# Performance work log

Hardware: AMD Instinct MI355X
Metric: run time of the kernel (lower is better)

## Reference

```python
import jax, jax.numpy as jnp
import numpy as np

EMBED_DIM = 128
NUM_SYMBOLS = 200000
B = 1024
K = 200
PROCESS_STEPS = 4


def setup_inputs() -> dict:
    key = jax.random.key(0)
    ks = jax.random.split(key, 10)
    D = EMBED_DIM
    emb = jax.random.normal(ks[0], (NUM_SYMBOLS + 1, D), jnp.float32) * 0.02
    emb = emb.at[NUM_SYMBOLS].set(0.0)  # padding_idx row
    return {
        "relations": jax.random.randint(ks[1], (B, K), 0, NUM_SYMBOLS),
        "entities": jax.random.randint(ks[2], (B, K), 0, NUM_SYMBOLS),
        "query": jax.random.randint(ks[3], (B,), 0, NUM_SYMBOLS),
        "symbol_emb": emb,
        "gcn_w_w": jax.random.normal(ks[4], (D, 2 * D), jnp.float32) / np.sqrt(2 * D).astype(np.float32),
        "gcn_w_b": jnp.zeros((D,), jnp.float32),
        "p1_w": jax.random.normal(ks[5], (2 * D, D), jnp.float32) / np.sqrt(D).astype(np.float32),
        "p1_b": jnp.zeros((2 * D,), jnp.float32),
        "p2_w": jax.random.normal(ks[6], (D, 2 * D), jnp.float32) / np.sqrt(2 * D).astype(np.float32),
        "p2_b": jnp.zeros((D,), jnp.float32),
        "ln_a": jnp.ones((D,), jnp.float32),
        "ln_b": jnp.zeros((D,), jnp.float32),
        "w_ih": jax.random.normal(ks[7], (8 * D, D), jnp.float32) * 0.05,
        "w_hh": jax.random.normal(ks[8], (8 * D, 2 * D), jnp.float32) * 0.05,
        "b_ih": jnp.zeros((8 * D,), jnp.float32),
        "b_hh": jnp.zeros((8 * D,), jnp.float32),
    }


def _layer_norm(z, a, b, eps=1e-3):
    # repo's LayerNormalization: (z - mu) / (std + eps) * a + b, unbiased std
    mu = jnp.mean(z, axis=-1, keepdims=True)
    sigma = jnp.std(z, axis=-1, ddof=1, keepdims=True)
    return (z - mu) / (sigma + eps) * a + b


def _forward(symbol_emb, gcn_w_w, gcn_w_b, p1_w, p1_b, p2_w, p2_b,
             ln_a, ln_b, w_ih, w_hh, b_ih, b_hh,
             relations, entities, query):
    D = symbol_emb.shape[1]
    # --- neighbor_encoder: gather -> concat -> linear -> neighbor sum -> tanh
    rel_e = symbol_emb[relations]                       # (B, K, D)
    ent_e = symbol_emb[entities]                        # (B, K, D)
    concat = jnp.concatenate([rel_e, ent_e], axis=-1)   # (B, K, 2D)
    out = jnp.einsum('bkf,df->bkd', concat, gcn_w_w) + gcn_w_b
    num_neighbors = jnp.asarray(relations.shape[0], out.dtype)  # code uses relations.size()[0]
    support = jnp.tanh(out.sum(axis=1) / num_neighbors)  # (B, D)
    # --- SupportEncoder: FFN with residual + layernorm (dropout off in eval)
    hidden = jax.nn.relu(support @ p1_w.T + p1_b)        # (B, 2D)
    support_g = _layer_norm(hidden @ p2_w.T + p2_b + support, ln_a, ln_b)
    # --- QueryEncoder: LSTMCell(D, 2D) process block with attention over support
    q = symbol_emb[query]                                # (B, D)
    bsz = q.shape[0]
    h_r = jnp.zeros((bsz, 2 * D), q.dtype)
    c = jnp.zeros((bsz, 2 * D), q.dtype)
    h_out = q
    for _ in range(PROCESS_STEPS):
        gates = q @ w_ih.T + b_ih + h_r @ w_hh.T + b_hh  # (B, 8D)
        i, f, g, o = jnp.split(gates, 4, axis=-1)
        c = jax.nn.sigmoid(f) * c + jax.nn.sigmoid(i) * jnp.tanh(g)
        h_ = jax.nn.sigmoid(o) * jnp.tanh(c)             # (B, 2D)
        h_out = q + h_[:, :D]                            # (B, D)
        attn = jax.nn.softmax(h_out @ support_g.T, axis=1)  # (B, B)
        r = attn @ support_g                             # (B, D)
        h_r = jnp.concatenate([h_out, r], axis=-1)       # (B, 2D)
    query_embeds = h_out
    # --- cosine similarity over dim=1
    cross = jnp.sum(query_embeds * support_g, axis=1)
    n1 = jnp.sum(query_embeds * query_embeds, axis=1)
    n2 = jnp.sum(support_g * support_g, axis=1)
    return cross / jnp.sqrt(n1 * n2)                     # (B,)


def reference(relations, entities, query, symbol_emb, gcn_w_w, gcn_w_b,
              p1_w, p1_b, p2_w, p2_b, ln_a, ln_b, w_ih, w_hh, b_ih, b_hh):
    return _forward(symbol_emb, gcn_w_w, gcn_w_b, p1_w, p1_b, p2_w, p2_b,
                    ln_a, ln_b, w_ih, w_hh, b_ih, b_hh,
                    relations, entities, query)
```

## Files before the change

### kernel.cpp

```cpp
#include <hip/hip_runtime.h>
#include <math.h>

#define D 128
#define B_SZ 1024
#define KNB 200
#define AHW 392
#define PW 1048

typedef _Float16 half8 __attribute__((ext_vector_type(8)));
typedef float floatx4 __attribute__((ext_vector_type(4)));

__device__ __forceinline__ float sigmoid_f(float x) { return 1.f / (1.f + __expf(-x)); }
__device__ __forceinline__ float tanh_fast(float x) { return 1.f - 2.f / (__expf(2.f * x) + 1.f); }

__device__ __forceinline__ half8 h8zero() {
    half8 z;
    #pragma unroll
    for (int i = 0; i < 8; ++i) z[i] = (_Float16)0.f;
    return z;
}

__global__ __launch_bounds__(512) void k_support(
    const int* __restrict__ relations, const int* __restrict__ entities,
    const int* __restrict__ query, const float* __restrict__ emb,
    const float* __restrict__ gcn_w, const float* __restrict__ gcn_b,
    const float* __restrict__ p1_w, const float* __restrict__ p1_b,
    const float* __restrict__ p2_w, const float* __restrict__ p2_b,
    const float* __restrict__ ln_a, const float* __restrict__ ln_b,
    const float* __restrict__ w_ih, const float* __restrict__ w_hh,
    _Float16* __restrict__ w16,
    float* __restrict__ sg, _Float16* __restrict__ sgH, _Float16* __restrict__ sgT,
    float* __restrict__ qb, _Float16* __restrict__ qbH)
{
    __shared__ int idxs[2 * KNB];
    __shared__ __align__(16) float part[16][132];
    __shared__ __align__(16) float S[2 * D];
    __shared__ __align__(16) float sup[D];
    __shared__ __align__(16) float hid[2 * D];
    __shared__ __align__(16) float zv[D];
    __shared__ float red2[2];

    const int b = blockIdx.x;
    const int t = threadIdx.x;

    if (b < 96) {
        const int i8 = (b * 512 + t) * 8;
        const float* src = (i8 < 131072) ? (w_ih + i8) : (w_hh + (i8 - 131072));
        float4 v0 = *(const float4*)src;
        float4 v1 = *(const float4*)(src + 4);
        half8 h;
        h[0] = (_Float16)v0.x; h[1] = (_Float16)v0.y; h[2] = (_Float16)v0.z; h[3] = (_Float16)v0.w;
        h[4] = (_Float16)v1.x; h[5] = (_Float16)v1.y; h[6] = (_Float16)v1.z; h[7] = (_Float16)v1.w;
        *(half8*)&w16[i8] = h;
    }

    if (t < KNB) idxs[t] = relations[b * KNB + t];
    else if (t < 2 * KNB) idxs[t] = entities[b * KNB + (t - KNB)];
    __syncthreads();

    {
        const int g = t >> 5, c4 = (t & 31) * 4;
        const int* mi = &idxs[(g >> 3) * KNB];
        float4 a4 = make_float4(0.f, 0.f, 0.f, 0.f);
        #pragma unroll 5
        for (int k = (g & 7); k < KNB; k += 8) {
            float4 v = *(const float4*)&emb[(size_t)mi[k] * D + c4];
            a4.x += v.x; a4.y += v.y; a4.z += v.z; a4.w += v.w;
        }
        *(float4*)&part[g][c4] = a4;
    }
    __syncthreads();
    if (t < 2 * D) {
        const int half = t >> 7, c = t & 127;
        float s = 0.f;
        #pragma unroll
        for (int j = 0; j < 8; ++j) s += part[half * 8 + j][c];
        S[t] = s;
    }
    __syncthreads();

    if (t < D) {
        const float4* w4 = (const float4*)(gcn_w + t * 2 * D);
        float dot = 0.f;
        #pragma unroll 8
        for (int f = 0; f < 2 * D / 4; ++f) {
            float4 w = w4[f];
            float4 s = *(const float4*)&S[f * 4];
            dot += w.x * s.x + w.y * s.y + w.z * s.z + w.w * s.w;
        }
        float v = (dot + 200.f * gcn_b[t]) * (1.f / 1024.f);
        sup[t] = tanhf(v);
    }
    __syncthreads();

    if (t < 2 * D) {
        const float4* w4 = (const float4*)(p1_w + t * D);
        float dot = 0.f;
        #pragma unroll 8
        for (int f = 0; f < D / 4; ++f) {
            float4 w = w4[f];
            float4 s = *(const float4*)&sup[f * 4];
            dot += w.x * s.x + w.y * s.y + w.z * s.z + w.w * s.w;
        }
        float h = dot + p1_b[t];
        hid[t] = h > 0.f ? h : 0.f;
    }
    __syncthreads();

    if (t < D) {
        const float4* w4 = (const float4*)(p2_w + t * 2 * D);
        float dot = 0.f;
        #pragma unroll 8
        for (int f = 0; f < 2 * D / 4; ++f) {
            float4 w = w4[f];
            float4 s = *(const float4*)&hid[f * 4];
            dot += w.x * s.x + w.y * s.y + w.z * s.z + w.w * s.w;
        }
        zv[t] = dot + p2_b[t] + sup[t];
    }
    __syncthreads();

    if (t < 64) {
        float x0 = zv[t], x1 = zv[t + 64];
        float s = x0 + x1;
        for (int off = 32; off; off >>= 1) s += __shfl_down(s, off);
        float mu = __shfl(s, 0) * (1.f / 128.f);
        float d0 = x0 - mu, d1 = x1 - mu;
        float v = d0 * d0 + d1 * d1;
        for (int off = 32; off; off >>= 1) v += __shfl_down(v, off);
        v = __shfl(v, 0);
        if (t == 0) { red2[0] = mu; red2[1] = sqrtf(v * (1.f / 127.f)); }
    }
    __syncthreads();
    if (t < D) {
        float mu = red2[0], sigma = red2[1];
        float val = (zv[t] - mu) / (sigma + 1e-3f) * ln_a[t] + ln_b[t];
        sg[b * D + t] = val;
        sgH[b * D + t] = (_Float16)val;
        sgT[t * B_SZ + b] = (_Float16)val;
        float qv = emb[(size_t)query[b] * D + t];
        qb[b * D + t] = qv;
        qbH[b * D + t] = (_Float16)qv;
    }
}

__global__ __launch_bounds__(512)
void k_lstm(
    const _Float16* __restrict__ qbH, const float* __restrict__ qb,
    const _Float16* __restrict__ sgH, const _Float16* __restrict__ sgT,
    const float* __restrict__ sg, const _Float16* __restrict__ w16,
    const float* __restrict__ b_ih, const float* __restrict__ b_hh,
    float* __restrict__ out)
{
    __shared__ _Float16 Ah[16 * AHW];
    __shared__ _Float16 P[16 * PW];
    __shared__ float qF[8][132];
    __shared__ float hF[8][132];
    __shared__ float pm[8][12];
    __shared__ float ps[8][12];

    const int t = threadIdx.x;
    const int w = t >> 6, lane = t & 63;
    const int m = lane & 15, quad = lane >> 4;
    const int b0 = blockIdx.x * 8;

    for (int i = t; i < 16 * AHW / 8; i += 512) *(half8*)&Ah[i * 8] = h8zero();
    for (int i = t; i < 8 * PW / 8; i += 512) *(half8*)&P[8 * PW + i * 8] = h8zero();
    __syncthreads();
    if (t < 128) {
        const int row = t >> 4, c = (t & 15) * 8;
        *(half8*)&Ah[row * AHW + c] = *(const half8*)&qbH[(size_t)(b0 + row) * D + c];
    }
    if (t < 256) {
        const int row = t >> 5, c = (t & 31) * 4;
        *(float4*)&qF[row][c] = *(const float4*)&qb[(size_t)(b0 + row) * D + c];
    }
    __syncthreads();

    float cregA[4] = {0.f, 0.f, 0.f, 0.f};
    float cregB[4] = {0.f, 0.f, 0.f, 0.f};

    #pragma unroll 1
    for (int s = 0; s < 4; ++s) {
        if (s > 0) {
            floatx4 a2[8];
            #pragma unroll
            for (int i = 0; i < 8; ++i)
                #pragma unroll
                for (int z = 0; z < 4; ++z) a2[i][z] = 0.f;
            #pragma unroll 1
            for (int ks = 0; ks < 4; ++ks) {
                half8 a = *(const half8*)&Ah[m * AHW + 128 + ks * 32 + quad * 8];
                const _Float16* sb = sgH + (size_t)m * D + ks * 32 + quad * 8;
                #pragma unroll
                for (int g4 = 0; g4 < 2; ++g4) {
                    half8 b0v = *(const half8*)(sb + (size_t)((w * 8 + g4 * 4 + 0) * 16) * D);
                    half8 b1v = *(const half8*)(sb + (size_t)((w * 8 + g4 * 4 + 1) * 16) * D);
                    half8 b2v = *(const half8*)(sb + (size_t)((w * 8 + g4 * 4 + 2) * 16) * D);
                    half8 b3v = *(const half8*)(sb + (size_t)((w * 8 + g4 * 4 + 3) * 16) * D);
                    a2[g4 * 4 + 0] = __builtin_amdgcn_mfma_f32_16x16x32_f16(a, b0v, a2[g4 * 4 + 0], 0, 0, 0);
                    a2[g4 * 4 + 1] = __builtin_amdgcn_mfma_f32_16x16x32_f16(a, b1v, a2[g4 * 4 + 1], 0, 0, 0);
                    a2[g4 * 4 + 2] = __builtin_amdgcn_mfma_f32_16x16x32_f16(a, b2v, a2[g4 * 4 + 2], 0, 0, 0);
                    a2[g4 * 4 + 3] = __builtin_amdgcn_mfma_f32_16x16x32_f16(a, b3v, a2[g4 * 4 + 3], 0, 0, 0);
                }
            }

            float mx[4];
            #pragma unroll
            for (int rr = 0; rr < 4; ++rr) {
                float v0 = fmaxf(fmaxf(a2[0][rr], a2[1][rr]), fmaxf(a2[2][rr], a2[3][rr]));
                float v1 = fmaxf(fmaxf(a2[4][rr], a2[5][rr]), fmaxf(a2[6][rr], a2[7][rr]));
                mx[rr] = fmaxf(v0, v1);
            }
            #pragma unroll
            for (int off = 1; off <= 8; off <<= 1)
                #pragma unroll
                for (int rr = 0; rr < 4; ++rr)
                    mx[rr] = fmaxf(mx[rr], __shfl_xor(mx[rr], off));
            if (m == 0) {
                #pragma unroll
                for (int rr = 0; rr < 4; ++rr) {
                    const int row = quad * 4 + rr;
                    if (row < 8) pm[w][row] = mx[rr];
                }
            }
            __syncthreads();

            float gm[4];
            #pragma unroll
            for (int rr = 0; rr < 4; ++rr) {
                const int row = quad * 4 + rr;
                float mm = -1e30f;
                if (row < 8) {
                    #pragma unroll
                    for (int ww = 0; ww < 8; ++ww) mm = fmaxf(mm, pm[ww][row]);
                }
                gm[rr] = mm;
            }
            float sl[4] = {0.f, 0.f, 0.f, 0.f};
            #pragma unroll
            for (int i = 0; i < 8; ++i) {
                const int col = (w * 8 + i) * 16 + m;
                #pragma unroll
                for (int rr = 0; rr < 4; ++rr) {
                    const int row = quad * 4 + rr;
                    if (row < 8) {
                        float e = __expf(a2[i][rr] - gm[rr]);
                        P[row * PW + col] = (_Float16)e;
                        sl[rr] += e;
                    }
                }
            }
            #pragma unroll
            for (int off = 1; off <= 8; off <<= 1)
                #pragma unroll
                for (int rr = 0; rr < 4; ++rr)
                    sl[rr] += __shfl_xor(sl[rr], off);
            if (m == 0) {
                #pragma unroll
                for (int rr = 0; rr < 4; ++rr) {
                    const int row = quad * 4 + rr;
                    if (row < 8) ps[w][row] = sl[rr];
                }
            }
            __syncthreads();

            float sinvd[4];
            #pragma unroll
            for (int rr = 0; rr < 4; ++rr) {
                const int row = quad * 4 + rr;
                float ss = 1.f;
                if (row < 8) {
                    ss = 0.f;
                    #pragma unroll
                    for (int ww = 0; ww < 8; ++ww) ss += ps[ww][row];
                }
                sinvd[rr] = 1.f / ss;
            }

            {
                floatx4 a3;
                #pragma unroll
                for (int z = 0; z < 4; ++z) a3[z] = 0.f;
                const _Float16* tb = sgT + (size_t)(w * 16 + m) * B_SZ + quad * 8;
                half8 c0 = *(const half8*)(tb);
                half8 c1 = *(const half8*)(tb + 32);
                #pragma unroll 1
                for (int ks = 0; ks < 32; ++ks) {
                    half8 nx = c1;
                    if (ks < 30) nx = *(const half8*)(tb + (ks + 2) * 32);
                    half8 a = *(const half8*)&P[m * PW + ks * 32 + quad * 8];
                    a3 = __builtin_amdgcn_mfma_f32_16x16x32_f16(a, c0, a3, 0, 0, 0);
                    c0 = c1; c1 = nx;
                }
                #pragma unroll
                for (int rr = 0; rr < 4; ++rr) {
                    const int row = quad * 4 + rr;
                    if (row < 8)
                        Ah[row * AHW + 256 + w * 16 + m] = (_Float16)(a3[rr] * sinvd[rr]);
                }
            }
            __syncthreads();
        }

        float hreg[4] = {0.f, 0.f, 0.f, 0.f};
        auto gates_half = [&](int v, float* cregH, bool wantH) {
            floatx4 acc[4];
            #pragma unroll
            for (int g = 0; g < 4; ++g) {
                floatx4 ac;
                #pragma unroll
                for (int z = 0; z < 4; ++z) ac[z] = 0.f;
                const _Float16* wb0 = w16 + (size_t)(g * 256 + v * 16 + m) * 128 + quad * 8;
                const _Float16* wb1 = w16 + 131072 + (size_t)(g * 256 + v * 16 + m) * 256 + quad * 8;
                half8 cur = *(const half8*)wb0;
                #pragma unroll 1
                for (int ks = 0; ks < 12; ++ks) {
                    half8 nxt = cur;
                    if (ks < 3)       nxt = *(const half8*)(wb0 + (ks + 1) * 32);
                    else if (ks < 11) nxt = *(const half8*)(wb1 + (ks - 3) * 32);
                    half8 a = *(const half8*)&Ah[m * AHW + ks * 32 + quad * 8];
                    ac = __builtin_amdgcn_mfma_f32_16x16x32_f16(a, cur, ac, 0, 0, 0);
                    cur = nxt;
                }
                acc[g] = ac;
            }
            const int unit = v * 16 + m;
            float bi0 = b_ih[unit] + b_hh[unit];
            float bi1 = b_ih[256 + unit] + b_hh[256 + unit];
            float bi2 = b_ih[512 + unit] + b_hh[512 + unit];
            float bi3 = b_ih[768 + unit] + b_hh[768 + unit];
            #pragma unroll
            for (int rr = 0; rr < 4; ++rr) {
                float gi = acc[0][rr] + bi0;
                float gf = acc[1][rr] + bi1;
                float gg = acc[2][rr] + bi2;
                float go = acc[3][rr] + bi3;
                float cn = sigmoid_f(gf) * cregH[rr] + sigmoid_f(gi) * tanh_fast(gg);
                cregH[rr] = cn;
                if (wantH) hreg[rr] = sigmoid_f(go) * tanh_fast(cn);
            }
        };
        gates_half(w, cregA, true);
        gates_half(w + 8, cregB, false);
        __syncthreads();

        {
            const int unit = w * 16 + m;
            #pragma unroll
            for (int rr = 0; rr < 4; ++rr) {
                const int row = quad * 4 + rr;
                if (row < 8) {
                    float ho = qF[row][unit] + hreg[rr];
                    Ah[row * AHW + 128 + unit] = (_Float16)ho;
                    hF[row][unit] = ho;
                }
            }
        }
        __syncthreads();
    }

    {
        const int row = w;
        float a0 = hF[row][lane], a1 = hF[row][lane + 64];
        float s0 = sg[(size_t)(b0 + row) * D + lane], s1 = sg[(size_t)(b0 + row) * D + lane + 64];
        float cr = a0 * s0 + a1 * s1;
        float n1 = a0 * a0 + a1 * a1;
        float n2 = s0 * s0 + s1 * s1;
        for (int off = 32; off; off >>= 1) {
            cr += __shfl_down(cr, off);
            n1 += __shfl_down(n1, off);
            n2 += __shfl_down(n2, off);
        }
        if (lane == 0) out[b0 + row] = cr / sqrtf(n1 * n2);
    }
}

extern "C" void kernel_launch(void* const* d_in, const int* in_sizes, int n_in,
                              void* d_out, int out_size, void* d_ws, size_t ws_size,
                              hipStream_t stream)
{
    const int*   relations = (const int*)d_in[0];
    const int*   entities  = (const int*)d_in[1];
    const int*   query     = (const int*)d_in[2];
    const float* emb       = (const float*)d_in[3];
    const float* gcn_w     = (const float*)d_in[4];
    const float* gcn_b     = (const float*)d_in[5];
    const float* p1_w      = (const float*)d_in[6];
    const float* p1_b      = (const float*)d_in[7];
    const float* p2_w      = (const float*)d_in[8];
    const float* p2_b      = (const float*)d_in[9];
    const float* ln_a      = (const float*)d_in[10];
    const float* ln_b      = (const float*)d_in[11];
    const float* w_ih      = (const float*)d_in[12];
    const float* w_hh      = (const float*)d_in[13];
    const float* b_ih      = (const float*)d_in[14];
    const float* b_hh      = (const float*)d_in[15];

    float* ws = (float*)d_ws;
    float*     sg   = ws;
    float*     qb   = ws + 131072;
    _Float16*  sgH  = (_Float16*)(ws + 262144);
    _Float16*  sgT  = (_Float16*)(ws + 327680);
    _Float16*  qbH  = (_Float16*)(ws + 393216);
    _Float16*  w16  = (_Float16*)(ws + 458752);

    k_support<<<dim3(B_SZ), dim3(512), 0, stream>>>(
        relations, entities, query, emb, gcn_w, gcn_b,
        p1_w, p1_b, p2_w, p2_b, ln_a, ln_b,
        w_ih, w_hh, w16,
        sg, sgH, sgT, qb, qbH);
    k_lstm<<<dim3(B_SZ / 8), dim3(512), 0, stream>>>(
        qbH, qb, sgH, sgT, sg, w16, b_ih, b_hh, (float*)d_out);
}
```

Before: 328.0 us.

## Interleave fused W_ih/W_hh weights and software-pipeline LSTM MFMA loops

The fp16 weight conversion now writes W_ih and W_hh rows interleaved into a single 384-wide row, so each gate row is read as one contiguous stream. The gate GEMM runs all 8 gate tiles together with double-buffered register prefetch, and biases and pointers are hoisted out of the step loop. The attention score GEMM and the P·S GEMM are restructured to keep several independent MFMA accumulators in flight with loads issued ahead. This hides global-memory latency on the serial LSTM recurrence, at the cost of higher register pressure; a waves_per_eu(2) hint is added to bound occupancy.

```diff
diff --git a/kernel.cpp b/kernel.cpp
--- a/kernel.cpp
+++ b/kernel.cpp
@@ -45,13 +45,24 @@
 
     if (b < 96) {
         const int i8 = (b * 512 + t) * 8;
-        const float* src = (i8 < 131072) ? (w_ih + i8) : (w_hh + (i8 - 131072));
+        const float* src;
+        _Float16* dst;
+        if (i8 < 131072) {
+            const int row = i8 >> 7, col = i8 & 127;
+            src = w_ih + i8;
+            dst = w16 + (size_t)row * 384 + col;
+        } else {
+            const int j = i8 - 131072;
+            const int row = j >> 8, col = j & 255;
+            src = w_hh + j;
+            dst = w16 + (size_t)row * 384 + 128 + col;
+        }
         float4 v0 = *(const float4*)src;
         float4 v1 = *(const float4*)(src + 4);
         half8 h;
         h[0] = (_Float16)v0.x; h[1] = (_Float16)v0.y; h[2] = (_Float16)v0.z; h[3] = (_Float16)v0.w;
         h[4] = (_Float16)v1.x; h[5] = (_Float16)v1.y; h[6] = (_Float16)v1.z; h[7] = (_Float16)v1.w;
-        *(half8*)&w16[i8] = h;
+        *(half8*)dst = h;
     }
 
     if (t < KNB) idxs[t] = relations[b * KNB + t];
@@ -145,6 +156,7 @@
 }
 
 __global__ __launch_bounds__(512)
+__attribute__((amdgpu_waves_per_eu(2)))
 void k_lstm(
     const _Float16* __restrict__ qbH, const float* __restrict__ qb,
     const _Float16* __restrict__ sgH, const _Float16* __restrict__ sgT,
@@ -175,33 +187,55 @@
         const int row = t >> 5, c = (t & 31) * 4;
         *(float4*)&qF[row][c] = *(const float4*)&qb[(size_t)(b0 + row) * D + c];
     }
-    __syncthreads();
 
     float cregA[4] = {0.f, 0.f, 0.f, 0.f};
     float cregB[4] = {0.f, 0.f, 0.f, 0.f};
+    float bi[8];
+    const _Float16* wp[8];
+    #pragma unroll
+    for (int c = 0; c < 8; ++c) {
+        const int unit = (w + (c >> 2) * 8) * 16 + m;
+        bi[c] = b_ih[(c & 3) * 256 + unit] + b_hh[(c & 3) * 256 + unit];
+        wp[c] = w16 + (size_t)((c & 3) * 256 + unit) * 384 + quad * 8;
+    }
+    __syncthreads();
 
     #pragma unroll 1
     for (int s = 0; s < 4; ++s) {
+        float sinvd[4] = {1.f, 1.f, 1.f, 1.f};
         if (s > 0) {
             floatx4 a2[8];
             #pragma unroll
             for (int i = 0; i < 8; ++i)
                 #pragma unroll
                 for (int z = 0; z < 4; ++z) a2[i][z] = 0.f;
-            #pragma unroll 1
-            for (int ks = 0; ks < 4; ++ks) {
-                half8 a = *(const half8*)&Ah[m * AHW + 128 + ks * 32 + quad * 8];
-                const _Float16* sb = sgH + (size_t)m * D + ks * 32 + quad * 8;
-                #pragma unroll
-                for (int g4 = 0; g4 < 2; ++g4) {
-                    half8 b0v = *(const half8*)(sb + (size_t)((w * 8 + g4 * 4 + 0) * 16) * D);
-                    half8 b1v = *(const half8*)(sb + (size_t)((w * 8 + g4 * 4 + 1) * 16) * D);
-                    half8 b2v = *(const half8*)(sb + (size_t)((w * 8 + g4 * 4 + 2) * 16) * D);
-                    half8 b3v = *(const half8*)(sb + (size_t)((w * 8 + g4 * 4 + 3) * 16) * D);
-                    a2[g4 * 4 + 0] = __builtin_amdgcn_mfma_f32_16x16x32_f16(a, b0v, a2[g4 * 4 + 0], 0, 0, 0);
-                    a2[g4 * 4 + 1] = __builtin_amdgcn_mfma_f32_16x16x32_f16(a, b1v, a2[g4 * 4 + 1], 0, 0, 0);
-                    a2[g4 * 4 + 2] = __builtin_amdgcn_mfma_f32_16x16x32_f16(a, b2v, a2[g4 * 4 + 2], 0, 0, 0);
-                    a2[g4 * 4 + 3] = __builtin_amdgcn_mfma_f32_16x16x32_f16(a, b3v, a2[g4 * 4 + 3], 0, 0, 0);
+            {
+                const _Float16* sp[8];
+                #pragma unroll
+                for (int i = 0; i < 8; ++i)
+                    sp[i] = sgH + (size_t)((w * 8 + i) * 16 + m) * D + quad * 8;
+                half8 sA[8], sB[8];
+                #pragma unroll
+                for (int i = 0; i < 8; ++i) sA[i] = *(const half8*)(sp[i]);
+                half8 a0 = *(const half8*)&Ah[m * AHW + 128 + quad * 8];
+                half8 a1;
+                #pragma unroll 1
+                for (int kk = 0; kk < 2; ++kk) {
+                    const int ks = kk * 2;
+                    #pragma unroll
+                    for (int i = 0; i < 8; ++i) sB[i] = *(const half8*)(sp[i] + (ks + 1) * 32);
+                    a1 = *(const half8*)&Ah[m * AHW + 128 + (ks + 1) * 32 + quad * 8];
+                    #pragma unroll
+                    for (int i = 0; i < 8; ++i)
+                        a2[i] = __builtin_amdgcn_mfma_f32_16x16x32_f16(a0, sA[i], a2[i], 0, 0, 0);
+                    if (kk < 1) {
+                        #pragma unroll
+                        for (int i = 0; i < 8; ++i) sA[i] = *(const half8*)(sp[i] + (ks + 2) * 32);
+                        a0 = *(const half8*)&Ah[m * AHW + 128 + (ks + 2) * 32 + quad * 8];
+                    }
+                    #pragma unroll
+                    for (int i = 0; i < 8; ++i)
+                        a2[i] = __builtin_amdgcn_mfma_f32_16x16x32_f16(a1, sB[i], a2[i], 0, 0, 0);
                 }
             }
 
@@ -265,7 +299,6 @@
             }
             __syncthreads();
 
-            float sinvd[4];
             #pragma unroll
             for (int rr = 0; rr < 4; ++rr) {
                 const int row = quad * 4 + rr;
@@ -279,70 +312,90 @@
             }
 
             {
-                floatx4 a3;
-                #pragma unroll
-                for (int z = 0; z < 4; ++z) a3[z] = 0.f;
                 const _Float16* tb = sgT + (size_t)(w * 16 + m) * B_SZ + quad * 8;
-                half8 c0 = *(const half8*)(tb);
-                half8 c1 = *(const half8*)(tb + 32);
+                const int pbase = m * PW + quad * 8;
+                floatx4 rc0, rc1, rc2, rc3;
+                #pragma unroll
+                for (int z = 0; z < 4; ++z) { rc0[z] = 0.f; rc1[z] = 0.f; rc2[z] = 0.f; rc3[z] = 0.f; }
+                half8 tA = *(const half8*)(tb);
+                half8 pA = *(const half8*)&P[pbase];
+                half8 tB = *(const half8*)(tb + 32);
+                half8 pB = *(const half8*)&P[pbase + 32];
+                half8 tC = *(const half8*)(tb + 64);
+                half8 pC = *(const half8*)&P[pbase + 64];
+                half8 tD = *(const half8*)(tb + 96);
+                half8 pD = *(const half8*)&P[pbase + 96];
                 #pragma unroll 1
-                for (int ks = 0; ks < 32; ++ks) {
-                    half8 nx = c1;
-                    if (ks < 30) nx = *(const half8*)(tb + (ks + 2) * 32);
-                    half8 a = *(const half8*)&P[m * PW + ks * 32 + quad * 8];
-                    a3 = __builtin_amdgcn_mfma_f32_16x16x32_f16(a, c0, a3, 0, 0, 0);
-                    c0 = c1; c1 = nx;
+                for (int kk = 0; kk < 8; ++kk) {
+                    const int ks = kk * 4;
+                    rc0 = __builtin_amdgcn_mfma_f32_16x16x32_f16(pA, tA, rc0, 0, 0, 0);
+                    if (kk < 7) { tA = *(const half8*)(tb + (ks + 4) * 32); pA = *(const half8*)&P[pbase + (ks + 4) * 32]; }
+                    rc1 = __builtin_amdgcn_mfma_f32_16x16x32_f16(pB, tB, rc1, 0, 0, 0);
+                    if (kk < 7) { tB = *(const half8*)(tb + (ks + 5) * 32); pB = *(const half8*)&P[pbase + (ks + 5) * 32]; }
+                    rc2 = __builtin_amdgcn_mfma_f32_16x16x32_f16(pC, tC, rc2, 0, 0, 0);
+                    if (kk < 7) { tC = *(const half8*)(tb + (ks + 6) * 32); pC = *(const half8*)&P[pbase + (ks + 6) * 32]; }
+                    rc3 = __builtin_amdgcn_mfma_f32_16x16x32_f16(pD, tD, rc3, 0, 0, 0);
+                    if (kk < 7) { tD = *(const half8*)(tb + (ks + 7) * 32); pD = *(const half8*)&P[pbase + (ks + 7) * 32]; }
                 }
                 #pragma unroll
                 for (int rr = 0; rr < 4; ++rr) {
                     const int row = quad * 4 + rr;
-                    if (row < 8)
-                        Ah[row * AHW + 256 + w * 16 + m] = (_Float16)(a3[rr] * sinvd[rr]);
+                    if (row < 8) {
+                        float rv = (rc0[rr] + rc1[rr] + rc2[rr] + rc3[rr]) * sinvd[rr];
+                        Ah[row * AHW + 256 + w * 16 + m] = (_Float16)rv;
+                    }
                 }
             }
             __syncthreads();
         }
 
-        float hreg[4] = {0.f, 0.f, 0.f, 0.f};
-        auto gates_half = [&](int v, float* cregH, bool wantH) {
-            floatx4 acc[4];
-            #pragma unroll
-            for (int g = 0; g < 4; ++g) {
-                floatx4 ac;
-                #pragma unroll
-                for (int z = 0; z < 4; ++z) ac[z] = 0.f;
-                const _Float16* wb0 = w16 + (size_t)(g * 256 + v * 16 + m) * 128 + quad * 8;
-                const _Float16* wb1 = w16 + 131072 + (size_t)(g * 256 + v * 16 + m) * 256 + quad * 8;
-                half8 cur = *(const half8*)wb0;
-                #pragma unroll 1
-                for (int ks = 0; ks < 12; ++ks) {
-                    half8 nxt = cur;
-                    if (ks < 3)       nxt = *(const half8*)(wb0 + (ks + 1) * 32);
-                    else if (ks < 11) nxt = *(const half8*)(wb1 + (ks - 3) * 32);
-                    half8 a = *(const half8*)&Ah[m * AHW + ks * 32 + quad * 8];
-                    ac = __builtin_amdgcn_mfma_f32_16x16x32_f16(a, cur, ac, 0, 0, 0);
-                    cur = nxt;
-                }
-                acc[g] = ac;
-            }
-            const int unit = v * 16 + m;
-            float bi0 = b_ih[unit] + b_hh[unit];
-            float bi1 = b_ih[256 + unit] + b_hh[256 + unit];
-            float bi2 = b_ih[512 + unit] + b_hh[512 + unit];
-            float bi3 = b_ih[768 + unit] + b_hh[768 + unit];
-            #pragma unroll
-            for (int rr = 0; rr < 4; ++rr) {
-                float gi = acc[0][rr] + bi0;
-                float gf = acc[1][rr] + bi1;
-                float gg = acc[2][rr] + bi2;
-                float go = acc[3][rr] + bi3;
-                float cn = sigmoid_f(gf) * cregH[rr] + sigmoid_f(gi) * tanh_fast(gg);
-                cregH[rr] = cn;
-                if (wantH) hreg[rr] = sigmoid_f(go) * tanh_fast(cn);
-            }
-        };
-        gates_half(w, cregA, true);
-        gates_half(w + 8, cregB, false);
+        floatx4 acc[8];
+        #pragma unroll
+        for (int c = 0; c < 8; ++c)
+            #pragma unroll
+            for (int z = 0; z < 4; ++z) acc[c][z] = 0.f;
+        {
+            half8 wA[8], wB[8];
+            #pragma unroll
+            for (int c = 0; c < 8; ++c) wA[c] = *(const half8*)(wp[c]);
+            half8 a0 = *(const half8*)&Ah[m * AHW + quad * 8];
+            half8 a1;
+            #pragma unroll 1
+            for (int kk = 0; kk < 6; ++kk) {
+                const int ks = kk * 2;
+                #pragma unroll
+                for (int c = 0; c < 8; ++c) wB[c] = *(const half8*)(wp[c] + (ks + 1) * 32);
+                a1 = *(const half8*)&Ah[m * AHW + (ks + 1) * 32 + quad * 8];
+                #pragma unroll
+                for (int c = 0; c < 8; ++c)
+                    acc[c] = __builtin_amdgcn_mfma_f32_16x16x32_f16(a0, wA[c], acc[c], 0, 0, 0);
+                if (kk < 5) {
+                    #pragma unroll
+                    for (int c = 0; c < 8; ++c) wA[c] = *(const half8*)(wp[c] + (ks + 2) * 32);
+                    a0 = *(const half8*)&Ah[m * AHW + (ks + 2) * 32 + quad * 8];
+                }
+                #pragma unroll
+                for (int c = 0; c < 8; ++c)
+                    acc[c] = __builtin_amdgcn_mfma_f32_16x16x32_f16(a1, wB[c], acc[c], 0, 0, 0);
+            }
+        }
+
+        float hregA[4];
+        #pragma unroll
+        for (int rr = 0; rr < 4; ++rr) {
+            float gi = acc[0][rr] + bi[0];
+            float gf = acc[1][rr] + bi[1];
+            float gg = acc[2][rr] + bi[2];
+            float go = acc[3][rr] + bi[3];
+            float cn = sigmoid_f(gf) * cregA[rr] + sigmoid_f(gi) * tanh_fast(gg);
+            cregA[rr] = cn;
+            hregA[rr] = sigmoid_f(go) * tanh_fast(cn);
+            float gi1 = acc[4][rr] + bi[4];
+            float gf1 = acc[5][rr] + bi[5];
+            float gg1 = acc[6][rr] + bi[6];
+            float cn1 = sigmoid_f(gf1) * cregB[rr] + sigmoid_f(gi1) * tanh_fast(gg1);
+            cregB[rr] = cn1;
+        }
         __syncthreads();
 
         {
@@ -351,7 +404,7 @@
             for (int rr = 0; rr < 4; ++rr) {
                 const int row = quad * 4 + rr;
                 if (row < 8) {
-                    float ho = qF[row][unit] + hreg[rr];
+                    float ho = qF[row][unit] + hregA[rr];
                     Ah[row * AHW + 128 + unit] = (_Float16)ho;
                     hF[row][unit] = ho;
                 }
```

After: 362.7 us. 10.6% more time.
